# Performance work log

Hardware: AMD Instinct MI355X
Metric: run time of the kernel (lower is better)

The kernel has to match this reference:

```python
import jax, jax.numpy as jnp
import numpy as np

N_BATCH, D_FEAT, GROUPS = 16384, 4096, 32


def _dct2(x):
    # torch_dct.dct with norm=None: unnormalized DCT-II via FFT, scaled by 2
    N = x.shape[-1]
    v = jnp.concatenate([x[..., ::2], x[..., 1::2][..., ::-1]], axis=-1)
    Vc = jnp.fft.fft(v, axis=-1)
    k = -jnp.arange(N, dtype=x.dtype) * (np.pi / (2.0 * N))
    return 2.0 * (Vc.real * jnp.cos(k) - Vc.imag * jnp.sin(k))


def _idct2(X):
    # torch_dct.idct with norm=None: inverse of _dct2 (scaled DCT-III via iFFT)
    N = X.shape[-1]
    Xv = X / 2.0
    k = jnp.arange(N, dtype=X.dtype) * (np.pi / (2.0 * N))
    W_r, W_i = jnp.cos(k), jnp.sin(k)
    Vt_i = jnp.concatenate([jnp.zeros_like(Xv[..., :1]), -Xv[..., ::-1][..., :-1]], axis=-1)
    V = jax.lax.complex(Xv * W_r - Vt_i * W_i, Xv * W_i + Vt_i * W_r)
    v = jnp.fft.ifft(V, axis=-1).real
    x = jnp.zeros_like(v)
    x = x.at[..., ::2].set(v[..., : N - N // 2])
    x = x.at[..., 1::2].set(v[..., ::-1][..., : N // 2])
    return x


def _gconv(x, W):
    # grouped 1x1 conv on [n, d] == block-diagonal matmul; W: [g, out_pg, in_pg]
    n, d = x.shape
    g, o, i = W.shape
    return jnp.einsum('ngi,goi->ngo', x.reshape(n, g, i), W).reshape(n, d)


def _riffle(x):
    n, d = x.shape
    return x.reshape(n, d // 2, 2).transpose(0, 2, 1).reshape(n, d)


def setup_inputs() -> dict:
    key = jax.random.key(0)
    k1, k2, k3, k4 = jax.random.split(key, 4)
    cpg = D_FEAT // GROUPS
    return {
        'x': jax.random.normal(k1, (N_BATCH, D_FEAT), dtype=jnp.float32),
        'A': jax.random.normal(k2, (GROUPS, cpg, cpg), dtype=jnp.float32) * (1.0 / np.sqrt(cpg)),
        'D': jax.random.normal(k3, (GROUPS, cpg, cpg), dtype=jnp.float32) * (1.0 / np.sqrt(cpg)),
        'bias': jax.random.uniform(k4, (1, D_FEAT), dtype=jnp.float32,
                                   minval=-1.0 / np.sqrt(D_FEAT), maxval=1.0 / np.sqrt(D_FEAT)),
    }


def reference(x, A, D, bias):
    y = _gconv(x, A)
    y = _dct2(y)
    y = _gconv(y, D)
    y = _idct2(y)
    y = _riffle(y)
    return y + bias
```

## Files before the change

### kernel.cpp

```cpp
#include <hip/hip_runtime.h>
#include <hip/hip_bf16.h>
#include <stdint.h>


typedef __attribute__((ext_vector_type(8))) short bf16x8;
typedef __attribute__((ext_vector_type(4))) float f32x4;

static __device__ __forceinline__ unsigned short f2bf(float f) {
    union { float f; unsigned u; } v; v.f = f;
    unsigned r = v.u + 0x7FFFu + ((v.u >> 16) & 1u);
    return (unsigned short)(r >> 16);
}

__global__ void k_cvt4(const float* __restrict__ in, unsigned short* __restrict__ out) {
    long long i = ((long long)blockIdx.x * 256 + threadIdx.x) * 4;
    float4 v = *(const float4*)(in + i);
    ushort4 o;
    o.x = f2bf(v.x); o.y = f2bf(v.y); o.z = f2bf(v.z); o.w = f2bf(v.w);
    *(ushort4*)(out + i) = o;
}

__global__ void k_cvt_At(const float* __restrict__ A, unsigned short* __restrict__ At) {
    int idx = blockIdx.x * 256 + threadIdx.x;
    int g = idx >> 14, o = (idx >> 7) & 127, i = idx & 127;
    At[(g << 14) + (i << 7) + o] = f2bf(A[idx]);
}

__global__ void k_gen_c2(unsigned short* __restrict__ C2) {
    int idx = blockIdx.x * 256 + threadIdx.x;
    int k = idx >> 12, j = idx & 4095;
    int m = (k * (2 * j + 1)) & 16383;
    float c = __cosf((float)m * 3.8349519697141029e-4f);
    C2[idx] = f2bf(2.0f * c);
}

__global__ void k_gen_c3(unsigned short* __restrict__ C3) {
    int idx = blockIdx.x * 256 + threadIdx.x;
    int j = idx >> 12, k = idx & 4095;
    int m = (k * (2 * j + 1)) & 16383;
    float c = __cosf((float)m * 3.8349519697141029e-4f);
    float w = (k == 0) ? 0.5f : 1.0f;
    C3[idx] = f2bf(c * w * (1.0f / 4096.0f));
}

template<int MODE>
__global__ __launch_bounds__(256) void k_gemm(
    const unsigned short* __restrict__ Aop, int lda, long long aGS,
    const unsigned short* __restrict__ Bop, int ldb, long long bGS,
    void* __restrict__ Cop, int ldc, long long cGS,
    int K, const float* __restrict__ bias)
{
    __shared__ unsigned short As[128 * 32];
    __shared__ unsigned short Bs[128 * 32];
    const int t = threadIdx.x;
    const int lane = t & 63;
    const int wave = t >> 6;
    const int wr = wave >> 1, wc = wave & 1;
    const int g = blockIdx.z;

    const unsigned short* Ap = Aop + (long long)g * aGS + (long long)blockIdx.y * 128 * lda;
    const unsigned short* Bp = Bop + (long long)g * bGS + (long long)blockIdx.x * 128 * ldb;

    const int srow = t >> 2;
    const int scol = (t & 3) * 8;
    unsigned short* ldsA = As + wave * 512;
    unsigned short* ldsB = Bs + wave * 512;

    f32x4 acc[4][4] = {};

    for (int k0 = 0; k0 < K; k0 += 32) {
        __syncthreads();
        #pragma unroll
        for (int h = 0; h < 2; ++h) {
            const unsigned short* ga = Ap + (long long)(h * 64 + srow) * lda + (k0 + scol);
            const unsigned short* gb = Bp + (long long)(h * 64 + srow) * ldb + (k0 + scol);
            __builtin_amdgcn_global_load_lds(
                (const __attribute__((address_space(1))) void*)ga,
                (__attribute__((address_space(3))) void*)(ldsA + h * 2048), 16, 0, 0);
            __builtin_amdgcn_global_load_lds(
                (const __attribute__((address_space(1))) void*)gb,
                (__attribute__((address_space(3))) void*)(ldsB + h * 2048), 16, 0, 0);
        }
        __syncthreads();

        const int fr = lane & 15, fq = lane >> 4;
        bf16x8 a[4], b[4];
        #pragma unroll
        for (int m = 0; m < 4; ++m)
            a[m] = *(const bf16x8*)(As + (wr * 64 + m * 16 + fr) * 32 + fq * 8);
        #pragma unroll
        for (int n = 0; n < 4; ++n)
            b[n] = *(const bf16x8*)(Bs + (wc * 64 + n * 16 + fr) * 32 + fq * 8);
        #pragma unroll
        for (int m = 0; m < 4; ++m)
            #pragma unroll
            for (int n = 0; n < 4; ++n)
                acc[m][n] = __builtin_amdgcn_mfma_f32_16x16x32_bf16(a[m], b[n], acc[m][n], 0, 0, 0);
    }

    const int fr = lane & 15, fq = lane >> 4;
    const int rowB = blockIdx.y * 128 + wr * 64;
    const int colB = blockIdx.x * 128 + wc * 64;

    if (MODE == 0) {
        unsigned short* C = (unsigned short*)Cop + (long long)g * cGS;
        #pragma unroll
        for (int m = 0; m < 4; ++m)
        #pragma unroll
        for (int n = 0; n < 4; ++n) {
            int crow = colB + n * 16 + fr;
            int ccol = rowB + m * 16 + fq * 4;
            ushort4 p;
            p.x = f2bf(acc[m][n][0]); p.y = f2bf(acc[m][n][1]);
            p.z = f2bf(acc[m][n][2]); p.w = f2bf(acc[m][n][3]);
            *(ushort4*)(C + (long long)crow * ldc + ccol) = p;
        }
    }
}

template<int MODE>
__global__ __launch_bounds__(512, 2) void k_gemm256(
    const unsigned short* __restrict__ Aop, int lda,
    const unsigned short* __restrict__ Bop, int ldb,
    void* __restrict__ Cop, int ldc,
    int K, int nbx, const float* __restrict__ bias)
{
    __shared__ unsigned short smem[65536];
    const int tid  = threadIdx.x;
    const int lane = tid & 63;
    const int wave = tid >> 6;
    const int wr = wave >> 2, wc = wave & 3;
    const int fr = lane & 15, fq = lane >> 4;

    const int nwg = gridDim.x;
    const int bid = blockIdx.x;
    const int swz = (bid & 7) * (nwg >> 3) + (bid >> 3);
    const int bx = swz % nbx, by = swz / nbx;

    const unsigned short* Ap = Aop + (long long)by * 256 * lda;
    const unsigned short* Bp = Bop + (long long)bx * 256 * ldb;

    const int srow = tid >> 3;
    const int scol = ((tid & 7) ^ (srow & 7)) << 3;
    const unsigned short* aSrc = Ap + (long long)srow * lda + scol;
    const unsigned short* bSrc = Bp + (long long)srow * ldb + scol;

    const char* sm = (const char*)smem;
    const int aB0 = wr * 16384 + fr * 128;
    const int bB0 = 32768 + (wc >> 1) * 16384 + (wc & 1) * 8192 + fr * 128;
    const int swz0 = ((fq) ^ (fr & 7)) << 4;
    const int swz1 = ((4 + fq) ^ (fr & 7)) << 4;

    f32x4 acc[8][4] = {};
    bf16x8 af[2][4][2];
    bf16x8 bb[2][2][2];

#define STAGE(SRC, LD, H, K0, LDSS)                                            \
    _Pragma("unroll")                                                          \
    for (int j = 0; j < 2; ++j)                                                \
        __builtin_amdgcn_global_load_lds(                                      \
            (const __attribute__((address_space(1))) void*)(SRC + (long long)((H) * 128 + j * 64) * (LD) + (K0)), \
            (__attribute__((address_space(3))) void*)(smem + (LDSS) + j * 4096 + wave * 512), \
            16, 0, 0);

#define READ_A(MH, BO)                                                         \
    _Pragma("unroll")                                                          \
    for (int i = 0; i < 4; ++i) {                                              \
        af[MH][i][0] = *(const bf16x8*)(sm + (BO) + aB0 + ((MH) * 4 + i) * 2048 + swz0); \
        af[MH][i][1] = *(const bf16x8*)(sm + (BO) + aB0 + ((MH) * 4 + i) * 2048 + swz1); \
    }

#define READ_B(NH, BO)                                                         \
    _Pragma("unroll")                                                          \
    for (int jj = 0; jj < 2; ++jj) {                                           \
        bb[NH][jj][0] = *(const bf16x8*)(sm + (BO) + bB0 + ((NH) * 2 + jj) * 2048 + swz0); \
        bb[NH][jj][1] = *(const bf16x8*)(sm + (BO) + bB0 + ((NH) * 2 + jj) * 2048 + swz1); \
    }

#define MFMA_Q(MH, NH)                                                         \
    __builtin_amdgcn_s_setprio(1);                                             \
    _Pragma("unroll")                                                          \
    for (int i = 0; i < 4; ++i)                                                \
        _Pragma("unroll")                                                      \
        for (int jj = 0; jj < 2; ++jj) {                                       \
            acc[(MH) * 4 + i][(NH) * 2 + jj] = __builtin_amdgcn_mfma_f32_16x16x32_bf16(af[MH][i][0], bb[NH][jj][0], acc[(MH) * 4 + i][(NH) * 2 + jj], 0, 0, 0); \
            acc[(MH) * 4 + i][(NH) * 2 + jj] = __builtin_amdgcn_mfma_f32_16x16x32_bf16(af[MH][i][1], bb[NH][jj][1], acc[(MH) * 4 + i][(NH) * 2 + jj], 0, 0, 0); \
        }                                                                      \
    __builtin_amdgcn_s_setprio(0);

#define BAR asm volatile("s_barrier" ::: "memory")

    STAGE(aSrc, lda, 0, 0, 0)
    STAGE(aSrc, lda, 1, 0, 8192)
    STAGE(bSrc, ldb, 0, 0, 16384)
    STAGE(bSrc, ldb, 1, 0, 24576)

    const int nt = K >> 6;
    for (int t = 0; t < nt; ++t) {
        const int bo = (t & 1) << 16;
        const int ns = ((t + 1) & 1) << 15;
        const int k1 = (t + 1) << 6;
        const bool hn = (t + 1) < nt;

        asm volatile("s_waitcnt vmcnt(0)" ::: "memory");
        BAR;

        if (hn) {
            STAGE(aSrc, lda, 0, k1, ns)
            STAGE(aSrc, lda, 1, k1, ns + 8192)
            STAGE(bSrc, ldb, 0, k1, ns + 16384)
            STAGE(bSrc, ldb, 1, k1, ns + 24576)
        }

        READ_A(0, bo)
        READ_B(0, bo)
        READ_B(1, bo)
        READ_A(1, bo)

        MFMA_Q(0, 0)
        MFMA_Q(0, 1)
        MFMA_Q(1, 1)
        MFMA_Q(1, 0)
    }
#undef STAGE
#undef READ_A
#undef READ_B
#undef MFMA_Q
#undef BAR

    const int rB = by * 256 + wr * 128 + fq * 4;
    const int cB = bx * 256 + wc * 64 + fr;
    if (MODE == 0) {
        unsigned short* C = (unsigned short*)Cop;
        #pragma unroll
        for (int m = 0; m < 8; ++m)
        #pragma unroll
        for (int n = 0; n < 4; ++n)
        #pragma unroll
        for (int q = 0; q < 4; ++q) {
            int r = rB + m * 16 + q;
            int rr = (r & 1) ? (2048 + (r >> 1)) : (r >> 1);
            C[(long long)rr * ldc + cB + n * 16] = f2bf(acc[m][n][q]);
        }
    } else {
        float* C = (float*)Cop;
        #pragma unroll
        for (int n = 0; n < 4; ++n) {
            float bv = bias[cB + n * 16];
            #pragma unroll
            for (int m = 0; m < 8; ++m)
            #pragma unroll
            for (int q = 0; q < 4; ++q)
                C[(long long)(rB + m * 16 + q) * ldc + cB + n * 16] = acc[m][n][q] + bv;
        }
    }
}

extern "C" void kernel_launch(void* const* d_in, const int* in_sizes, int n_in,
                              void* d_out, int out_size, void* d_ws, size_t ws_size,
                              hipStream_t stream) {
    const float* x    = (const float*)d_in[0];
    const float* Af   = (const float*)d_in[1];
    const float* Dfm  = (const float*)d_in[2];
    const float* bias = (const float*)d_in[3];
    float* out = (float*)d_out;
    char* ws = (char*)d_ws;

    unsigned short* Xbf = (unsigned short*)(ws);
    unsigned short* B1  = (unsigned short*)(ws + 134217728ULL);
    unsigned short* B2  = (unsigned short*)(ws + 134217728ULL + 33554432ULL);
    unsigned short* B3  = (unsigned short*)(ws + 134217728ULL + 67108864ULL);
    unsigned short* Atb = (unsigned short*)(ws + 134217728ULL + 100663296ULL);
    unsigned short* Dtb = Atb + 524288;

    k_cvt4  <<<65536, 256, 0, stream>>>(x, Xbf);
    k_cvt4  <<<512,   256, 0, stream>>>(Dfm, Dtb);
    k_cvt_At<<<2048,  256, 0, stream>>>(Af, Atb);
    k_gen_c2<<<65536, 256, 0, stream>>>(B1);
    k_gen_c3<<<65536, 256, 0, stream>>>(B2);

    k_gemm<0><<<dim3(1, 32, 32), 256, 0, stream>>>(
        B1, 4096, 128LL,  Atb, 128, 16384LL,  B3, 4096, 524288LL, 128, nullptr);

    k_gemm<0><<<dim3(32, 1, 32), 256, 0, stream>>>(
        Dtb, 128, 16384LL,  B3, 4096, 128LL,  B1, 4096, 128LL, 128, nullptr);

    k_gemm256<0><<<256, 512, 0, stream>>>(B2, 4096, B1, 4096, B3, 4096, 4096, 16, nullptr);

    k_gemm256<1><<<1024, 512, 0, stream>>>(Xbf, 4096, B3, 4096, out, 4096, 4096, 16, bias);
}
```

Measured before the change: 746.7 us.

## Restructure GEMM main loop into an 8-phase ping-pong pipeline with interleaved staging

Replaces the simple double-buffered K loop, which waited for all global-to-LDS loads with vmcnt(0) at every step, with a two-tile unrolled schedule. LDS fragment reads, global_load_lds issues and MFMA quadrants are interleaved across eight barrier-separated phases, using partial vmcnt waits and per-phase lgkmcnt waits. The LDS staging layout also changes to per-thread contiguous slots with 64-row halves. Fragment registers are reused per quadrant, which lowers register pressure. The price is many more barriers and fragile correctness that depends on buffer slot reuse timing and on nt being even.

```diff
diff --git a/kernel.cpp b/kernel.cpp
--- a/kernel.cpp
+++ b/kernel.cpp
@@ -146,35 +146,36 @@
     const unsigned short* bSrc = Bp + (long long)srow * ldb + scol;
 
     const char* sm = (const char*)smem;
-    const int aB0 = wr * 16384 + fr * 128;
-    const int bB0 = 32768 + (wc >> 1) * 16384 + (wc & 1) * 8192 + fr * 128;
-    const int swz0 = ((fq) ^ (fr & 7)) << 4;
-    const int swz1 = ((4 + fq) ^ (fr & 7)) << 4;
+    const int aHB = wr * 16384;
+    const int bHB = 32768 + (wc >> 1) * 16384;
+    const int aR0 = fr * 128;
+    const int bR0 = ((wc & 1) * 64 + fr) * 128;
+    const int sw0 = (fq ^ (fr & 7)) << 4;
+    const int sw1 = ((4 + fq) ^ (fr & 7)) << 4;
 
     f32x4 acc[8][4] = {};
-    bf16x8 af[2][4][2];
-    bf16x8 bb[2][2][2];
-
-#define STAGE(SRC, LD, H, K0, LDSS)                                            \
+    bf16x8 af[4][2], bb[2][2];
+
+#define STG(SRC, LD, GR, K0, SLOT)                                             \
     _Pragma("unroll")                                                          \
     for (int j = 0; j < 2; ++j)                                                \
         __builtin_amdgcn_global_load_lds(                                      \
-            (const __attribute__((address_space(1))) void*)(SRC + (long long)((H) * 128 + j * 64) * (LD) + (K0)), \
-            (__attribute__((address_space(3))) void*)(smem + (LDSS) + j * 4096 + wave * 512), \
+            (const __attribute__((address_space(1))) void*)((SRC) + (long long)((GR) + j * 64) * (LD) + (K0)), \
+            (__attribute__((address_space(3))) void*)((char*)smem + (SLOT) + j * 8192 + tid * 16), \
             16, 0, 0);
 
 #define READ_A(MH, BO)                                                         \
     _Pragma("unroll")                                                          \
     for (int i = 0; i < 4; ++i) {                                              \
-        af[MH][i][0] = *(const bf16x8*)(sm + (BO) + aB0 + ((MH) * 4 + i) * 2048 + swz0); \
-        af[MH][i][1] = *(const bf16x8*)(sm + (BO) + aB0 + ((MH) * 4 + i) * 2048 + swz1); \
+        af[i][0] = *(const bf16x8*)(sm + (BO) + aHB + aR0 + ((MH) * 64 + i * 16) * 128 + sw0); \
+        af[i][1] = *(const bf16x8*)(sm + (BO) + aHB + aR0 + ((MH) * 64 + i * 16) * 128 + sw1); \
     }
 
 #define READ_B(NH, BO)                                                         \
     _Pragma("unroll")                                                          \
     for (int jj = 0; jj < 2; ++jj) {                                           \
-        bb[NH][jj][0] = *(const bf16x8*)(sm + (BO) + bB0 + ((NH) * 2 + jj) * 2048 + swz0); \
-        bb[NH][jj][1] = *(const bf16x8*)(sm + (BO) + bB0 + ((NH) * 2 + jj) * 2048 + swz1); \
+        bb[jj][0] = *(const bf16x8*)(sm + (BO) + bHB + bR0 + ((NH) * 2 + jj) * 2048 + sw0); \
+        bb[jj][1] = *(const bf16x8*)(sm + (BO) + bHB + bR0 + ((NH) * 2 + jj) * 2048 + sw1); \
     }
 
 #define MFMA_Q(MH, NH)                                                         \
@@ -183,50 +184,73 @@
     for (int i = 0; i < 4; ++i)                                                \
         _Pragma("unroll")                                                      \
         for (int jj = 0; jj < 2; ++jj) {                                       \
-            acc[(MH) * 4 + i][(NH) * 2 + jj] = __builtin_amdgcn_mfma_f32_16x16x32_bf16(af[MH][i][0], bb[NH][jj][0], acc[(MH) * 4 + i][(NH) * 2 + jj], 0, 0, 0); \
-            acc[(MH) * 4 + i][(NH) * 2 + jj] = __builtin_amdgcn_mfma_f32_16x16x32_bf16(af[MH][i][1], bb[NH][jj][1], acc[(MH) * 4 + i][(NH) * 2 + jj], 0, 0, 0); \
+            acc[(MH) * 4 + i][(NH) * 2 + jj] = __builtin_amdgcn_mfma_f32_16x16x32_bf16(af[i][0], bb[jj][0], acc[(MH) * 4 + i][(NH) * 2 + jj], 0, 0, 0); \
+            acc[(MH) * 4 + i][(NH) * 2 + jj] = __builtin_amdgcn_mfma_f32_16x16x32_bf16(af[i][1], bb[jj][1], acc[(MH) * 4 + i][(NH) * 2 + jj], 0, 0, 0); \
         }                                                                      \
     __builtin_amdgcn_s_setprio(0);
 
-#define BAR asm volatile("s_barrier" ::: "memory")
-
-    STAGE(aSrc, lda, 0, 0, 0)
-    STAGE(aSrc, lda, 1, 0, 8192)
-    STAGE(bSrc, ldb, 0, 0, 16384)
-    STAGE(bSrc, ldb, 1, 0, 24576)
+#define BAR   asm volatile("s_barrier" ::: "memory")
+#define LGKM0 asm volatile("s_waitcnt lgkmcnt(0)" ::: "memory")
+
+    STG(aSrc, lda, 0,   0, 0)
+    STG(aSrc, lda, 128, 0, 16384)
+    STG(bSrc, ldb, 0,   0, 32768)
+    STG(bSrc, ldb, 128, 0, 49152)
+    STG(aSrc, lda, 0,   64, 65536)
+    STG(aSrc, lda, 128, 64, 65536 + 16384)
+    STG(bSrc, ldb, 128, 64, 65536 + 49152)
+    asm volatile("s_waitcnt vmcnt(6)" ::: "memory");
+    BAR;
 
     const int nt = K >> 6;
-    for (int t = 0; t < nt; ++t) {
-        const int bo = (t & 1) << 16;
-        const int ns = ((t + 1) & 1) << 15;
-        const int k1 = (t + 1) << 6;
-        const bool hn = (t + 1) < nt;
-
-        asm volatile("s_waitcnt vmcnt(0)" ::: "memory");
-        BAR;
-
-        if (hn) {
-            STAGE(aSrc, lda, 0, k1, ns)
-            STAGE(aSrc, lda, 1, k1, ns + 8192)
-            STAGE(bSrc, ldb, 0, k1, ns + 16384)
-            STAGE(bSrc, ldb, 1, k1, ns + 24576)
-        }
-
-        READ_A(0, bo)
-        READ_B(0, bo)
-        READ_B(1, bo)
-        READ_A(1, bo)
-
-        MFMA_Q(0, 0)
-        MFMA_Q(0, 1)
-        MFMA_Q(1, 1)
-        MFMA_Q(1, 0)
-    }
-#undef STAGE
+    const int nit = nt >> 1;
+    for (int it = 0; it < nit; ++it) {
+        const int k1 = (2 * it + 1) << 6;
+        const int k2 = (2 * it + 2) << 6;
+        const int k3 = (2 * it + 3) << 6;
+        const bool s2 = (2 * it + 2) < nt;
+
+        READ_A(0, 0) READ_B(0, 0)
+        STG(bSrc, ldb, 0, k1, 65536 + 32768)
+        BAR; LGKM0; MFMA_Q(0, 0) BAR;
+        READ_B(1, 0)
+        BAR; LGKM0; MFMA_Q(0, 1) BAR;
+        READ_A(1, 0)
+        BAR; LGKM0; MFMA_Q(1, 1) BAR;
+        READ_B(0, 0)
+        if (s2) {
+            STG(aSrc, lda, 0,   k2, 0)
+            STG(aSrc, lda, 128, k2, 16384)
+            asm volatile("s_waitcnt vmcnt(4)" ::: "memory");
+        } else {
+            asm volatile("s_waitcnt vmcnt(0)" ::: "memory");
+        }
+        BAR; LGKM0; MFMA_Q(1, 0) BAR;
+        READ_A(0, 65536) READ_B(0, 65536)
+        if (s2) {
+            STG(bSrc, ldb, 128, k2, 49152)
+            STG(bSrc, ldb, 0,   k2, 32768)
+        }
+        BAR; LGKM0; MFMA_Q(0, 0) BAR;
+        READ_B(1, 65536)
+        BAR; LGKM0; MFMA_Q(0, 1) BAR;
+        READ_A(1, 65536)
+        BAR; LGKM0; MFMA_Q(1, 1) BAR;
+        READ_B(0, 65536)
+        if (s2) {
+            STG(aSrc, lda, 0,   k3, 65536)
+            STG(aSrc, lda, 128, k3, 65536 + 16384)
+            STG(bSrc, ldb, 128, k3, 65536 + 49152)
+            asm volatile("s_waitcnt vmcnt(6)" ::: "memory");
+        }
+        BAR; LGKM0; MFMA_Q(1, 0) BAR;
+    }
+#undef STG
 #undef READ_A
 #undef READ_B
 #undef MFMA_Q
 #undef BAR
+#undef LGKM0
 
     const int rB = by * 256 + wr * 128 + fq * 4;
     const int cB = bx * 256 + wc * 64 + fr;
```

After: 776.9 us. 1.04x slower.
